# Performance work log

Measured on AMD Instinct MI355X. Metric: run time of the kernel, lower is better.

The kernel has to match this reference:

```python
import jax, jax.numpy as jnp
import numpy as np

N = 50000   # nodes
R = 4       # relation groups
E = 800000  # nnz per relation adjacency
ED = 200000 # decoded edges
H = 128     # hidden_dim
L = 64      # latent_dim
DH = 64     # decoder_hidden_dim


def setup_inputs() -> dict:
    key = jax.random.key(0)
    ks = iter(jax.random.split(key, 64))
    def nrm(shape, scale=1.0):
        return jax.random.normal(next(ks), shape, dtype=jnp.float32) * scale
    inp = {}
    inp["x_process"] = nrm((N, 62))
    inp["x_file"] = nrm((N, 37))
    inp["x_network"] = nrm((N, 37))
    def lin(prefix, din, dout):
        s = 1.0 / np.sqrt(din)
        inp[prefix + "_Ws"] = nrm((dout, din), s)
        inp[prefix + "_bs"] = nrm((dout,), s)
        inp[prefix + "_Wr"] = nrm((R, dout, din), s)
        inp[prefix + "_br"] = nrm((R, dout), s)
    lin("p1", 62, H); lin("p2", H, L)
    lin("f1", 37, H); lin("f2", H, L)
    lin("n1", 37, H); lin("n2", H, L)
    inp["gate_W"] = nrm((3, L), 1.0 / np.sqrt(L))
    inp["gate_b"] = nrm((3,), 0.1)
    inp["dec_W1"] = nrm((DH, 4 * L), 1.0 / np.sqrt(4 * L))
    inp["dec_b1"] = nrm((DH,), 0.1)
    inp["dec_W2"] = nrm((1, DH), 1.0 / np.sqrt(DH))
    inp["dec_b2"] = nrm((1,), 0.1)
    inp["adj_rows"] = jax.random.randint(next(ks), (R, E), 0, N, dtype=jnp.int32)
    inp["adj_cols"] = jax.random.randint(next(ks), (R, E), 0, N, dtype=jnp.int32)
    inp["adj_vals"] = jax.random.uniform(next(ks), (R, E), dtype=jnp.float32) * 0.1
    inp["edge_src"] = jax.random.randint(next(ks), (ED,), 0, N, dtype=jnp.int32)
    inp["edge_dst"] = jax.random.randint(next(ks), (ED,), 0, N, dtype=jnp.int32)
    return inp


def reference(x_process, x_file, x_network,
              p1_Ws, p1_bs, p1_Wr, p1_br, p2_Ws, p2_bs, p2_Wr, p2_br,
              f1_Ws, f1_bs, f1_Wr, f1_br, f2_Ws, f2_bs, f2_Wr, f2_br,
              n1_Ws, n1_bs, n1_Wr, n1_br, n2_Ws, n2_bs, n2_Wr, n2_br,
              gate_W, gate_b, dec_W1, dec_b1, dec_W2, dec_b2,
              adj_rows, adj_cols, adj_vals, edge_src, edge_dst):
    def spmm(rows, cols, vals, x):  # A @ x, A in COO: out[row] += val * x[col]
        return jax.ops.segment_sum(vals[:, None] * x[cols], rows, num_segments=N)

    def rgcn_layer(x, Ws, bs, Wr, br):
        out = x @ Ws.T + bs  # self_linear
        for r in range(R):
            out = out + spmm(adj_rows[r], adj_cols[r], adj_vals[r], x) @ Wr[r].T + br[r]
        return out / float(R + 1)

    def encoder(x, W1s, b1s, W1r, b1r, W2s, b2s, W2r, b2r):
        h = jax.nn.relu(rgcn_layer(x, W1s, b1s, W1r, b1r))
        # dropout p=0.0 / eval mode -> identity
        return rgcn_layer(h, W2s, b2s, W2r, b2r)

    z_p = encoder(x_process, p1_Ws, p1_bs, p1_Wr, p1_br, p2_Ws, p2_bs, p2_Wr, p2_br)
    z_f = encoder(x_file, f1_Ws, f1_bs, f1_Wr, f1_br, f2_Ws, f2_bs, f2_Wr, f2_br)
    z_n = encoder(x_network, n1_Ws, n1_bs, n1_Wr, n1_br, n2_Ws, n2_bs, n2_Wr, n2_br)

    # gated multi-view fusion: three Linear(latent,1) gates -> softmax over views
    scores = jnp.stack([z_p @ gate_W[0] + gate_b[0],
                        z_f @ gate_W[1] + gate_b[1],
                        z_n @ gate_W[2] + gate_b[2]], axis=1)  # [N, 3]
    alpha = jax.nn.softmax(scores, axis=1)
    z = alpha[:, 0:1] * z_p + alpha[:, 1:2] * z_f + alpha[:, 2:3] * z_n  # [N, L]

    # mlp edge decoder
    zs = z[edge_src]
    zd = z[edge_dst]
    feats = jnp.concatenate([zs, zd, zs * zd, jnp.abs(zs - zd)], axis=1)  # [ED, 4L]
    hid = jax.nn.relu(feats @ dec_W1.T + dec_b1)
    logits = (hid @ dec_W2.T + dec_b2)[:, 0]  # [ED]
    return logits
```

## Files before the change

### kernel.cpp

```cpp
#include <hip/hip_runtime.h>

#define N_NODES 50000
#define R_REL   4
#define E_NNZ   800000
#define ED_EDGES 200000
#define H_DIM   128
#define L_DIM   64

#define RN_TOTAL (R_REL * N_NODES)
#define SCAN_BLK 196

#define WS_RP     0u
#define WS_CUR    800256u
#define WS_CNT    1600512u
#define WS_BSUM   2400512u
#define WS_CV     2401536u
#define WS_XALL   28001536u
#define WS_SP     47201536u
#define WS_SF     96801536u
#define WS_SN     126401536u
#define WS_HP     156001536u
#define WS_HF     181601536u
#define WS_HN     47201536u
#define WS_YSP    72801536u
#define WS_YRP    96801536u
#define WS_YSF    122401536u
#define WS_YRF    135201536u
#define WS_YSN    160801536u
#define WS_YRN    173601536u
#define WS_Z      199201536u

__device__ __forceinline__ ushort f2bf(float f) {
    unsigned u = __float_as_uint(f);
    unsigned r = (u + 0x7fffu + ((u >> 16) & 1u)) >> 16;
    return (ushort)r;
}
__device__ __forceinline__ float bf2f(ushort u) {
    return __uint_as_float(((unsigned)u) << 16);
}

__global__ void cast_xall_kernel(const float* __restrict__ xp, const float* __restrict__ xf,
                                 const float* __restrict__ xn, ushort* __restrict__ xall) {
    int i = blockIdx.x * 256 + threadIdx.x;
    if (i >= N_NODES * 192) return;
    int node = i / 192, k = i - node * 192;
    float v = 0.f;
    if (k < 62) v = xp[node * 62 + k];
    else if (k >= 64 && k < 138) {
        int j = k - 64, d = j >> 1;
        v = (j & 1) ? xn[node * 37 + d] : xf[node * 37 + d];
    }
    xall[i] = f2bf(v);
}

__global__ void zero_kernel(int* p, int n) {
    int i = blockIdx.x * blockDim.x + threadIdx.x;
    if (i < n) p[i] = 0;
}

__global__ void hist_kernel(const int* __restrict__ rows, int* __restrict__ counts) {
    int g = blockIdx.x * blockDim.x + threadIdx.x;
    if (g >= R_REL * E_NNZ) return;
    int r = g / E_NNZ;
    atomicAdd(&counts[r * N_NODES + rows[g]], 1);
}

__global__ void scan_part_kernel(const int* __restrict__ counts, int* __restrict__ bsum) {
    __shared__ int red[256];
    int base = blockIdx.x * 1024;
    int t = threadIdx.x;
    int s = 0;
    #pragma unroll
    for (int i = 0; i < 4; i++) {
        int idx = base + i * 256 + t;
        if (idx < RN_TOTAL) s += counts[idx];
    }
    red[t] = s; __syncthreads();
    for (int d = 128; d > 0; d >>= 1) {
        if (t < d) red[t] += red[t + d];
        __syncthreads();
    }
    if (t == 0) bsum[blockIdx.x] = red[0];
}

__global__ void scan_bsum_kernel(int* __restrict__ bsum, int* __restrict__ rp) {
    __shared__ int sh[256];
    int t = threadIdx.x;
    int v = (t < SCAN_BLK) ? bsum[t] : 0;
    sh[t] = v; __syncthreads();
    for (int d = 1; d < 256; d <<= 1) {
        int u = (t >= d) ? sh[t - d] : 0;
        __syncthreads();
        sh[t] += u;
        __syncthreads();
    }
    if (t < SCAN_BLK) bsum[t] = sh[t] - v;
    if (t == 255) rp[RN_TOTAL] = sh[255];
}

__global__ void scan_final_kernel(const int* __restrict__ counts, const int* __restrict__ bsum,
                                  int* __restrict__ rp, int* __restrict__ cursor) {
    __shared__ int sh[256];
    int base = blockIdx.x * 1024;
    int t = threadIdx.x;
    int c[4]; int s = 0;
    #pragma unroll
    for (int i = 0; i < 4; i++) {
        int idx = base + t * 4 + i;
        c[i] = (idx < RN_TOTAL) ? counts[idx] : 0;
        s += c[i];
    }
    sh[t] = s; __syncthreads();
    for (int d = 1; d < 256; d <<= 1) {
        int u = (t >= d) ? sh[t - d] : 0;
        __syncthreads();
        sh[t] += u;
        __syncthreads();
    }
    int off = bsum[blockIdx.x] + sh[t] - s;
    #pragma unroll
    for (int i = 0; i < 4; i++) {
        int idx = base + t * 4 + i;
        if (idx < RN_TOTAL) { rp[idx] = off; cursor[idx] = off; }
        off += c[i];
    }
}

__global__ void scatter_kernel(const int* __restrict__ rows, const int* __restrict__ cols,
                               const float* __restrict__ vals, int* __restrict__ cursor,
                               int2* __restrict__ cse) {
    int g = blockIdx.x * blockDim.x + threadIdx.x;
    if (g >= R_REL * E_NNZ) return;
    int r = g / E_NNZ;
    int p = atomicAdd(&cursor[r * N_NODES + rows[g]], 1);
    cse[p] = make_int2(cols[g], __float_as_int(vals[g]));
}

__global__ void spmm1_all_kernel(const ushort* __restrict__ xall,
                                 const int* __restrict__ rp, const int2* __restrict__ cse,
                                 float* __restrict__ Sp, float* __restrict__ Sf,
                                 float* __restrict__ Sn) {
    int wave = threadIdx.x >> 6, lane = threadIdx.x & 63;
    int row = blockIdx.x * 4 + wave;
    if (row >= N_NODES) return;
    bool lp = lane < 62, lf = lane < 37;
    int opx = lane;
    int ofn = 64 + 2 * lane;
    for (int r = 0; r < R_REL; r++) {
        int e0 = rp[r * N_NODES + row], e1 = rp[r * N_NODES + row + 1];
        float ap = 0.f, af = 0.f, an = 0.f;
        int e = e0;
        for (; e + 4 <= e1; e += 4) {
            int2 q0 = cse[e], q1 = cse[e + 1], q2 = cse[e + 2], q3 = cse[e + 3];
            const ushort* b0 = xall + (size_t)q0.x * 192;
            const ushort* b1 = xall + (size_t)q1.x * 192;
            const ushort* b2 = xall + (size_t)q2.x * 192;
            const ushort* b3 = xall + (size_t)q3.x * 192;
            ushort  p0 = b0[opx], p1 = b1[opx], p2 = b2[opx], p3 = b3[opx];
            ushort2 u0 = *(const ushort2*)&b0[ofn];
            ushort2 u1 = *(const ushort2*)&b1[ofn];
            ushort2 u2 = *(const ushort2*)&b2[ofn];
            ushort2 u3 = *(const ushort2*)&b3[ofn];
            float v0 = __int_as_float(q0.y), v1 = __int_as_float(q1.y);
            float v2 = __int_as_float(q2.y), v3 = __int_as_float(q3.y);
            ap += v0 * bf2f(p0) + v1 * bf2f(p1) + v2 * bf2f(p2) + v3 * bf2f(p3);
            af += v0 * bf2f(u0.x) + v1 * bf2f(u1.x) + v2 * bf2f(u2.x) + v3 * bf2f(u3.x);
            an += v0 * bf2f(u0.y) + v1 * bf2f(u1.y) + v2 * bf2f(u2.y) + v3 * bf2f(u3.y);
        }
        for (; e < e1; e++) {
            int2 q = cse[e];
            const ushort* b = xall + (size_t)q.x * 192;
            float v = __int_as_float(q.y);
            ap += v * bf2f(b[opx]);
            ushort2 u = *(const ushort2*)&b[ofn];
            af += v * bf2f(u.x);
            an += v * bf2f(u.y);
        }
        if (lp) Sp[row * 248 + r * 62 + lane] = ap;
        if (lf) { Sf[row * 148 + r * 37 + lane] = af; Sn[row * 148 + r * 37 + lane] = an; }
    }
}

__launch_bounds__(256)
__global__ void gemm1_kernel(const float* __restrict__ x, const float* __restrict__ S,
                             const float* __restrict__ Ws, const float* __restrict__ bs,
                             const float* __restrict__ Wr, const float* __restrict__ br,
                             float* __restrict__ h, int din) {
    __shared__ float sA[64 * 63];
    __shared__ float sW[62 * 132];
    int t = threadIdx.x;
    int i0 = blockIdx.x * 64;
    int rg = t >> 5, cg = t & 31;
    float acc[8][4] = {};
    for (int s = 0; s < 5; s++) {
        const float* Aptr; int astride;
        if (s == 0) { Aptr = x; astride = din; }
        else        { Aptr = S + (s - 1) * din; astride = 4 * din; }
        const float* Wp = (s == 0) ? Ws : (Wr + (s - 1) * H_DIM * din);
        __syncthreads();
        for (int idx = t; idx < 64 * din; idx += 256) {
            int rr = idx / din, k = idx - rr * din;
            int grow = i0 + rr;
            sA[rr * 63 + k] = (grow < N_NODES) ? Aptr[grow * astride + k] : 0.f;
        }
        for (int idx = t; idx < H_DIM * din; idx += 256) {
            int j = idx / din, k = idx - j * din;
            sW[k * 132 + j] = Wp[j * din + k];
        }
        __syncthreads();
        for (int k = 0; k < din; k++) {
            float a[8];
            #pragma unroll
            for (int rr = 0; rr < 8; rr++) a[rr] = sA[(rg * 8 + rr) * 63 + k];
            float4 w = *(const float4*)&sW[k * 132 + cg * 4];
            #pragma unroll
            for (int rr = 0; rr < 8; rr++) {
                acc[rr][0] += a[rr] * w.x; acc[rr][1] += a[rr] * w.y;
                acc[rr][2] += a[rr] * w.z; acc[rr][3] += a[rr] * w.w;
            }
        }
    }
    int j0 = cg * 4;
    float btot[4];
    #pragma unroll
    for (int cc = 0; cc < 4; cc++) {
        float b = bs[j0 + cc];
        #pragma unroll
        for (int r = 0; r < R_REL; r++) b += br[r * H_DIM + j0 + cc];
        btot[cc] = b;
    }
    #pragma unroll
    for (int rr = 0; rr < 8; rr++) {
        int grow = i0 + rg * 8 + rr;
        if (grow < N_NODES) {
            float4 o;
            o.x = fmaxf((acc[rr][0] + btot[0]) * 0.2f, 0.f);
            o.y = fmaxf((acc[rr][1] + btot[1]) * 0.2f, 0.f);
            o.z = fmaxf((acc[rr][2] + btot[2]) * 0.2f, 0.f);
            o.w = fmaxf((acc[rr][3] + btot[3]) * 0.2f, 0.f);
            *(float4*)&h[grow * H_DIM + j0] = o;
        }
    }
}

__launch_bounds__(256)
__global__ void gemm2_kernel(const float* __restrict__ h, const float* __restrict__ Ws2,
                             const float* __restrict__ Wr2, float* __restrict__ Yself,
                             ushort* __restrict__ Yrel) {
    __shared__ float sA[128 * 65];
    __shared__ float sW[64 * 68];
    int t = threadIdx.x;
    int i0 = blockIdx.x * 128;
    int ct = blockIdx.y;
    int rg = t >> 4, cg = t & 15;
    const float* Wp = (ct == 0) ? Ws2 : (Wr2 + (ct - 1) * 64 * H_DIM);
    float acc[8][4] = {};
    for (int kc = 0; kc < 2; kc++) {
        __syncthreads();
        for (int idx = t; idx < 128 * 64; idx += 256) {
            int rr = idx >> 6, k = idx & 63;
            int grow = i0 + rr;
            sA[rr * 65 + k] = (grow < N_NODES) ? h[grow * H_DIM + kc * 64 + k] : 0.f;
        }
        for (int idx = t; idx < 64 * 64; idx += 256) {
            int j = idx >> 6, k = idx & 63;
            sW[k * 68 + j] = Wp[j * H_DIM + kc * 64 + k];
        }
        __syncthreads();
        for (int k = 0; k < 64; k++) {
            float a[8];
            #pragma unroll
            for (int rr = 0; rr < 8; rr++) a[rr] = sA[(rg * 8 + rr) * 65 + k];
            float4 w = *(const float4*)&sW[k * 68 + cg * 4];
            #pragma unroll
            for (int rr = 0; rr < 8; rr++) {
                acc[rr][0] += a[rr] * w.x; acc[rr][1] += a[rr] * w.y;
                acc[rr][2] += a[rr] * w.z; acc[rr][3] += a[rr] * w.w;
            }
        }
    }
    #pragma unroll
    for (int rr = 0; rr < 8; rr++) {
        int grow = i0 + rg * 8 + rr;
        if (grow < N_NODES) {
            if (ct == 0) {
                float4 o = make_float4(acc[rr][0], acc[rr][1], acc[rr][2], acc[rr][3]);
                *(float4*)&Yself[(size_t)grow * 64 + cg * 4] = o;
            } else {
                ushort4 o;
                o.x = f2bf(acc[rr][0]); o.y = f2bf(acc[rr][1]);
                o.z = f2bf(acc[rr][2]); o.w = f2bf(acc[rr][3]);
                *(ushort4*)&Yrel[(size_t)grow * 256 + (ct - 1) * 64 + cg * 4] = o;
            }
        }
    }
}

__global__ void spmm2z_all_kernel(const float* __restrict__ Ysp, const ushort* __restrict__ Yrp,
                                  const float* __restrict__ Ysf, const ushort* __restrict__ Yrf,
                                  const float* __restrict__ Ysn, const ushort* __restrict__ Yrn,
                                  const int* __restrict__ rp, const int2* __restrict__ cse,
                                  const float* __restrict__ p_bs, const float* __restrict__ p_br,
                                  const float* __restrict__ f_bs, const float* __restrict__ f_br,
                                  const float* __restrict__ n_bs, const float* __restrict__ n_br,
                                  const float* __restrict__ gW, const float* __restrict__ gb,
                                  float* __restrict__ z) {
    int wave = threadIdx.x >> 6, lane = threadIdx.x & 63;
    int row = blockIdx.x * 4 + wave;
    if (row >= N_NODES) return;
    float aP = Ysp[(size_t)row * 64 + lane] + p_bs[lane]
             + p_br[lane] + p_br[64 + lane] + p_br[128 + lane] + p_br[192 + lane];
    float aF = Ysf[(size_t)row * 64 + lane] + f_bs[lane]
             + f_br[lane] + f_br[64 + lane] + f_br[128 + lane] + f_br[192 + lane];
    float aN = Ysn[(size_t)row * 64 + lane] + n_bs[lane]
             + n_br[lane] + n_br[64 + lane] + n_br[128 + lane] + n_br[192 + lane];
    for (int r = 0; r < R_REL; r++) {
        int e0 = rp[r * N_NODES + row], e1 = rp[r * N_NODES + row + 1];
        const ushort* yp = Yrp + r * 64 + lane;
        const ushort* yf = Yrf + r * 64 + lane;
        const ushort* yn = Yrn + r * 64 + lane;
        int e = e0;
        for (; e + 4 <= e1; e += 4) {
            int2 q0 = cse[e], q1 = cse[e + 1], q2 = cse[e + 2], q3 = cse[e + 3];
            size_t o0 = (size_t)q0.x * 256, o1 = (size_t)q1.x * 256;
            size_t o2 = (size_t)q2.x * 256, o3 = (size_t)q3.x * 256;
            float pp0 = bf2f(yp[o0]), pp1 = bf2f(yp[o1]), pp2 = bf2f(yp[o2]), pp3 = bf2f(yp[o3]);
            float ff0 = bf2f(yf[o0]), ff1 = bf2f(yf[o1]), ff2 = bf2f(yf[o2]), ff3 = bf2f(yf[o3]);
            float nn0 = bf2f(yn[o0]), nn1 = bf2f(yn[o1]), nn2 = bf2f(yn[o2]), nn3 = bf2f(yn[o3]);
            float v0 = __int_as_float(q0.y), v1 = __int_as_float(q1.y);
            float v2 = __int_as_float(q2.y), v3 = __int_as_float(q3.y);
            aP += v0 * pp0 + v1 * pp1 + v2 * pp2 + v3 * pp3;
            aF += v0 * ff0 + v1 * ff1 + v2 * ff2 + v3 * ff3;
            aN += v0 * nn0 + v1 * nn1 + v2 * nn2 + v3 * nn3;
        }
        for (; e < e1; e++) {
            int2 q = cse[e];
            size_t o = (size_t)q.x * 256;
            float v = __int_as_float(q.y);
            aP += v * bf2f(yp[o]);
            aF += v * bf2f(yf[o]);
            aN += v * bf2f(yn[o]);
        }
    }
    aP *= 0.2f; aF *= 0.2f; aN *= 0.2f;
    float sp = aP * gW[lane], sf = aF * gW[64 + lane], sn = aN * gW[128 + lane];
    #pragma unroll
    for (int d = 32; d >= 1; d >>= 1) {
        sp += __shfl_xor(sp, d);
        sf += __shfl_xor(sf, d);
        sn += __shfl_xor(sn, d);
    }
    sp += gb[0]; sf += gb[1]; sn += gb[2];
    float m = fmaxf(sp, fmaxf(sf, sn));
    float ep = __expf(sp - m), ef = __expf(sf - m), en = __expf(sn - m);
    float inv = 1.f / (ep + ef + en);
    z[row * 64 + lane] = (ep * aP + ef * aF + en * aN) * inv;
}

__launch_bounds__(256)
__global__ void decoder_kernel(const float* __restrict__ z, const int* __restrict__ esrc,
                               const int* __restrict__ edst, const float* __restrict__ w1,
                               const float* __restrict__ b1, const float* __restrict__ w2,
                               const float* __restrict__ b2, float* __restrict__ out) {
    int e = blockIdx.x * blockDim.x + threadIdx.x;
    if (e >= ED_EDGES) return;
    const float* zs = z + (size_t)esrc[e] * 64;
    const float* zd = z + (size_t)edst[e] * 64;
    float hid[64];
    #pragma unroll
    for (int j = 0; j < 64; j++) hid[j] = b1[j];
    #pragma unroll 1
    for (int kc = 0; kc < 64; kc += 8) {
        float a[8], b[8], p[8], q[8];
        #pragma unroll
        for (int kk = 0; kk < 8; kk++) {
            a[kk] = zs[kc + kk]; b[kk] = zd[kc + kk];
            p[kk] = a[kk] * b[kk]; q[kk] = fabsf(a[kk] - b[kk]);
        }
        #pragma unroll
        for (int j = 0; j < 64; j++) {
            const float* wrow = w1 + j * 256 + kc;
            float s = hid[j];
            #pragma unroll
            for (int kk = 0; kk < 8; kk++) {
                s += a[kk] * wrow[kk] + b[kk] * wrow[64 + kk]
                   + p[kk] * wrow[128 + kk] + q[kk] * wrow[192 + kk];
            }
            hid[j] = s;
        }
    }
    float logit = b2[0];
    #pragma unroll
    for (int j = 0; j < 64; j++) logit += fmaxf(hid[j], 0.f) * w2[j];
    out[e] = logit;
}

extern "C" void kernel_launch(void* const* d_in, const int* in_sizes, int n_in,
                              void* d_out, int out_size, void* d_ws, size_t ws_size,
                              hipStream_t stream) {
    const float* x_p = (const float*)d_in[0];
    const float* x_f = (const float*)d_in[1];
    const float* x_n = (const float*)d_in[2];
    const float* p1_Ws = (const float*)d_in[3];  const float* p1_bs = (const float*)d_in[4];
    const float* p1_Wr = (const float*)d_in[5];  const float* p1_br = (const float*)d_in[6];
    const float* p2_Ws = (const float*)d_in[7];  const float* p2_bs = (const float*)d_in[8];
    const float* p2_Wr = (const float*)d_in[9];  const float* p2_br = (const float*)d_in[10];
    const float* f1_Ws = (const float*)d_in[11]; const float* f1_bs = (const float*)d_in[12];
    const float* f1_Wr = (const float*)d_in[13]; const float* f1_br = (const float*)d_in[14];
    const float* f2_Ws = (const float*)d_in[15]; const float* f2_bs = (const float*)d_in[16];
    const float* f2_Wr = (const float*)d_in[17]; const float* f2_br = (const float*)d_in[18];
    const float* n1_Ws = (const float*)d_in[19]; const float* n1_bs = (const float*)d_in[20];
    const float* n1_Wr = (const float*)d_in[21]; const float* n1_br = (const float*)d_in[22];
    const float* n2_Ws = (const float*)d_in[23]; const float* n2_bs = (const float*)d_in[24];
    const float* n2_Wr = (const float*)d_in[25]; const float* n2_br = (const float*)d_in[26];
    const float* gate_W = (const float*)d_in[27]; const float* gate_b = (const float*)d_in[28];
    const float* dec_W1 = (const float*)d_in[29]; const float* dec_b1 = (const float*)d_in[30];
    const float* dec_W2 = (const float*)d_in[31]; const float* dec_b2 = (const float*)d_in[32];
    const int*   adj_rows = (const int*)d_in[33];
    const int*   adj_cols = (const int*)d_in[34];
    const float* adj_vals = (const float*)d_in[35];
    const int*   edge_src = (const int*)d_in[36];
    const int*   edge_dst = (const int*)d_in[37];

    char* ws = (char*)d_ws;
    int*    rp      = (int*)(ws + WS_RP);
    int*    cursor  = (int*)(ws + WS_CUR);
    int*    counts  = (int*)(ws + WS_CNT);
    int*    bsum    = (int*)(ws + WS_BSUM);
    int2*   cse     = (int2*)(ws + WS_CV);
    ushort* xall    = (ushort*)(ws + WS_XALL);
    float*  S_p = (float*)(ws + WS_SP);
    float*  S_f = (float*)(ws + WS_SF);
    float*  S_n = (float*)(ws + WS_SN);
    float*  h_p = (float*)(ws + WS_HP);
    float*  h_f = (float*)(ws + WS_HF);
    float*  h_n = (float*)(ws + WS_HN);
    float*  Ys_p = (float*)(ws + WS_YSP);  ushort* Yr_p = (ushort*)(ws + WS_YRP);
    float*  Ys_f = (float*)(ws + WS_YSF);  ushort* Yr_f = (ushort*)(ws + WS_YRF);
    float*  Ys_n = (float*)(ws + WS_YSN);  ushort* Yr_n = (ushort*)(ws + WS_YRN);
    float*  z   = (float*)(ws + WS_Z);
    float*  out = (float*)d_out;

    cast_xall_kernel<<<(N_NODES * 192 + 255) / 256, 256, 0, stream>>>(x_p, x_f, x_n, xall);

    zero_kernel<<<(RN_TOTAL + 255) / 256, 256, 0, stream>>>(counts, RN_TOTAL);
    hist_kernel<<<(R_REL * E_NNZ + 255) / 256, 256, 0, stream>>>(adj_rows, counts);
    scan_part_kernel<<<SCAN_BLK, 256, 0, stream>>>(counts, bsum);
    scan_bsum_kernel<<<1, 256, 0, stream>>>(bsum, rp);
    scan_final_kernel<<<SCAN_BLK, 256, 0, stream>>>(counts, bsum, rp, cursor);
    scatter_kernel<<<(R_REL * E_NNZ + 255) / 256, 256, 0, stream>>>(
        adj_rows, adj_cols, adj_vals, cursor, cse);

    spmm1_all_kernel<<<N_NODES / 4, 256, 0, stream>>>(xall, rp, cse, S_p, S_f, S_n);

    int g1 = (N_NODES + 63) / 64;
    gemm1_kernel<<<g1, 256, 0, stream>>>(x_p, S_p, p1_Ws, p1_bs, p1_Wr, p1_br, h_p, 62);
    gemm1_kernel<<<g1, 256, 0, stream>>>(x_f, S_f, f1_Ws, f1_bs, f1_Wr, f1_br, h_f, 37);
    gemm1_kernel<<<g1, 256, 0, stream>>>(x_n, S_n, n1_Ws, n1_bs, n1_Wr, n1_br, h_n, 37);

    dim3 g2((N_NODES + 127) / 128, 5);
    gemm2_kernel<<<g2, 256, 0, stream>>>(h_p, p2_Ws, p2_Wr, Ys_p, Yr_p);
    gemm2_kernel<<<g2, 256, 0, stream>>>(h_f, f2_Ws, f2_Wr, Ys_f, Yr_f);
    gemm2_kernel<<<g2, 256, 0, stream>>>(h_n, n2_Ws, n2_Wr, Ys_n, Yr_n);

    spmm2z_all_kernel<<<N_NODES / 4, 256, 0, stream>>>(
        Ys_p, Yr_p, Ys_f, Yr_f, Ys_n, Yr_n, rp, cse,
        p2_bs, p2_br, f2_bs, f2_br, n2_bs, n2_br, gate_W, gate_b, z);

    decoder_kernel<<<(ED_EDGES + 255) / 256, 256, 0, stream>>>(
        z, edge_src, edge_dst, dec_W1, dec_b1, dec_W2, dec_b2, out);
}
```

Measured before the change: 1.684 ms.

## Replace global-atomic COO-to-CSR build with two-pass LDS radix bucket sort

Builds the CSR adjacency with a two-level sort instead of global atomic histogram and scatter. The first pass buckets edges by relation and the high bits of the row using per-block shared-memory histograms. A prefix scan and scatter then fill a temp buffer, and a per-bucket kernel sorts by the low 8 row bits in LDS and writes row pointers and CSR entries. The aim is to cut contended global atomics and random scattered writes, at the cost of an extra pass through a temp buffer and more workspace aliasing.

```diff
diff --git a/kernel.cpp b/kernel.cpp
--- a/kernel.cpp
+++ b/kernel.cpp
@@ -8,27 +8,35 @@
 #define L_DIM   64
 
 #define RN_TOTAL (R_REL * N_NODES)
-#define SCAN_BLK 196
-
-#define WS_RP     0u
-#define WS_CUR    800256u
-#define WS_CNT    1600512u
-#define WS_BSUM   2400512u
-#define WS_CV     2401536u
-#define WS_XALL   28001536u
-#define WS_SP     47201536u
-#define WS_SF     96801536u
-#define WS_SN     126401536u
-#define WS_HP     156001536u
-#define WS_HF     181601536u
-#define WS_HN     47201536u
-#define WS_YSP    72801536u
-#define WS_YRP    96801536u
-#define WS_YSF    122401536u
-#define WS_YRF    135201536u
-#define WS_YSN    160801536u
-#define WS_YRN    173601536u
-#define WS_Z      199201536u
+#define ETOT     (R_REL * E_NNZ)
+
+#define EPB   8192
+#define NB    391
+#define RBK   196
+#define KBK   (R_REL * RBK)
+#define HTOT  (KBK * NB)
+#define SCB   300
+#define MAXB  6144
+
+#define WS_RP    0u
+#define WS_HIST  800256u
+#define WS_BSUM  2026496u
+#define WS_CV    2030592u
+#define WS_TMP   27630720u
+#define WS_XALL  53230720u
+#define WS_SP    72430720u
+#define WS_SF    122030720u
+#define WS_SN    151630720u
+#define WS_HPR   181230720u
+#define WS_HN    WS_TMP
+#define WS_HF    WS_SP
+#define WS_YSP   WS_XALL
+#define WS_YSF   (WS_SP + 25600000u)
+#define WS_YRP   WS_SF
+#define WS_YRF   WS_SN
+#define WS_YSN   WS_HPR
+#define WS_YRN   WS_HF
+#define WS_Z     194030720u
 
 __device__ __forceinline__ ushort f2bf(float f) {
     unsigned u = __float_as_uint(f);
@@ -53,27 +61,32 @@
     xall[i] = f2bf(v);
 }
 
-__global__ void zero_kernel(int* p, int n) {
-    int i = blockIdx.x * blockDim.x + threadIdx.x;
-    if (i < n) p[i] = 0;
-}
-
-__global__ void hist_kernel(const int* __restrict__ rows, int* __restrict__ counts) {
-    int g = blockIdx.x * blockDim.x + threadIdx.x;
-    if (g >= R_REL * E_NNZ) return;
-    int r = g / E_NNZ;
-    atomicAdd(&counts[r * N_NODES + rows[g]], 1);
-}
-
-__global__ void scan_part_kernel(const int* __restrict__ counts, int* __restrict__ bsum) {
+__global__ void radix_hist_kernel(const int* __restrict__ rows, int* __restrict__ H) {
+    __shared__ int hist[KBK];
+    int blk = blockIdx.x, t = threadIdx.x;
+    for (int i = t; i < KBK; i += 256) hist[i] = 0;
+    __syncthreads();
+    int base = blk * EPB;
+    #pragma unroll 1
+    for (int i = 0; i < EPB / 256; i++) {
+        int g = base + i * 256 + t;
+        if (g < ETOT) {
+            int r = g / E_NNZ;
+            atomicAdd(&hist[r * RBK + (rows[g] >> 8)], 1);
+        }
+    }
+    __syncthreads();
+    for (int i = t; i < KBK; i += 256) H[i * NB + blk] = hist[i];
+}
+
+__global__ void scan_part_kernel(const int* __restrict__ H, int* __restrict__ bsum) {
     __shared__ int red[256];
-    int base = blockIdx.x * 1024;
-    int t = threadIdx.x;
+    int base = blockIdx.x * 1024, t = threadIdx.x;
     int s = 0;
     #pragma unroll
     for (int i = 0; i < 4; i++) {
         int idx = base + i * 256 + t;
-        if (idx < RN_TOTAL) s += counts[idx];
+        if (idx < HTOT) s += H[idx];
     }
     red[t] = s; __syncthreads();
     for (int d = 128; d > 0; d >>= 1) {
@@ -84,30 +97,28 @@
 }
 
 __global__ void scan_bsum_kernel(int* __restrict__ bsum, int* __restrict__ rp) {
+    __shared__ int sh[512];
+    int t = threadIdx.x;
+    int v = (t < SCB) ? bsum[t] : 0;
+    sh[t] = v; __syncthreads();
+    for (int d = 1; d < 512; d <<= 1) {
+        int u = (t >= d) ? sh[t - d] : 0;
+        __syncthreads();
+        sh[t] += u;
+        __syncthreads();
+    }
+    if (t < SCB) bsum[t] = sh[t] - v;
+    if (t == 0) rp[RN_TOTAL] = ETOT;
+}
+
+__global__ void scan_final_kernel(int* __restrict__ H, const int* __restrict__ bsum) {
     __shared__ int sh[256];
-    int t = threadIdx.x;
-    int v = (t < SCAN_BLK) ? bsum[t] : 0;
-    sh[t] = v; __syncthreads();
-    for (int d = 1; d < 256; d <<= 1) {
-        int u = (t >= d) ? sh[t - d] : 0;
-        __syncthreads();
-        sh[t] += u;
-        __syncthreads();
-    }
-    if (t < SCAN_BLK) bsum[t] = sh[t] - v;
-    if (t == 255) rp[RN_TOTAL] = sh[255];
-}
-
-__global__ void scan_final_kernel(const int* __restrict__ counts, const int* __restrict__ bsum,
-                                  int* __restrict__ rp, int* __restrict__ cursor) {
-    __shared__ int sh[256];
-    int base = blockIdx.x * 1024;
-    int t = threadIdx.x;
+    int base = blockIdx.x * 1024, t = threadIdx.x;
     int c[4]; int s = 0;
     #pragma unroll
     for (int i = 0; i < 4; i++) {
         int idx = base + t * 4 + i;
-        c[i] = (idx < RN_TOTAL) ? counts[idx] : 0;
+        c[i] = (idx < HTOT) ? H[idx] : 0;
         s += c[i];
     }
     sh[t] = s; __syncthreads();
@@ -121,19 +132,71 @@
     #pragma unroll
     for (int i = 0; i < 4; i++) {
         int idx = base + t * 4 + i;
-        if (idx < RN_TOTAL) { rp[idx] = off; cursor[idx] = off; }
+        if (idx < HTOT) H[idx] = off;
         off += c[i];
     }
 }
 
-__global__ void scatter_kernel(const int* __restrict__ rows, const int* __restrict__ cols,
-                               const float* __restrict__ vals, int* __restrict__ cursor,
-                               int2* __restrict__ cse) {
-    int g = blockIdx.x * blockDim.x + threadIdx.x;
-    if (g >= R_REL * E_NNZ) return;
-    int r = g / E_NNZ;
-    int p = atomicAdd(&cursor[r * N_NODES + rows[g]], 1);
-    cse[p] = make_int2(cols[g], __float_as_int(vals[g]));
+__global__ void radix_scatter_kernel(const int* __restrict__ rows, const int* __restrict__ cols,
+                                     const float* __restrict__ vals, const int* __restrict__ H,
+                                     int2* __restrict__ tmp) {
+    __shared__ int cur[KBK];
+    int blk = blockIdx.x, t = threadIdx.x;
+    for (int i = t; i < KBK; i += 256) cur[i] = H[i * NB + blk];
+    __syncthreads();
+    int base = blk * EPB;
+    #pragma unroll 1
+    for (int i = 0; i < EPB / 256; i++) {
+        int g = base + i * 256 + t;
+        if (g < ETOT) {
+            int r = g / E_NNZ;
+            int row = rows[g];
+            int b = r * RBK + (row >> 8);
+            int p = atomicAdd(&cur[b], 1);
+            tmp[p] = make_int2(cols[g] | ((row & 255) << 16), __float_as_int(vals[g]));
+        }
+    }
+}
+
+__launch_bounds__(256)
+__global__ void bucket_sort_kernel(const int2* __restrict__ tmp, const int* __restrict__ H,
+                                   int* __restrict__ rp, int2* __restrict__ cse) {
+    __shared__ int hist[256];
+    __shared__ int sc[256];
+    __shared__ int cur[256];
+    __shared__ int2 eb[MAXB];
+    int b = blockIdx.x, t = threadIdx.x;
+    int start = H[b * NB];
+    int end = (b == KBK - 1) ? ETOT : H[(b + 1) * NB];
+    int cnt = end - start;
+    bool useLds = (cnt <= MAXB);
+    hist[t] = 0;
+    __syncthreads();
+    for (int i = t; i < cnt; i += 256) {
+        int2 e = tmp[start + i];
+        if (useLds) eb[i] = e;
+        atomicAdd(&hist[(e.x >> 16) & 255], 1);
+    }
+    __syncthreads();
+    sc[t] = hist[t]; __syncthreads();
+    for (int d = 1; d < 256; d <<= 1) {
+        int v = (t >= d) ? sc[t - d] : 0;
+        __syncthreads();
+        sc[t] += v;
+        __syncthreads();
+    }
+    int pref = sc[t] - hist[t];
+    int r = b / RBK, rh = b - r * RBK;
+    int grow = rh * 256 + t;
+    if (grow < N_NODES) rp[r * N_NODES + grow] = start + pref;
+    cur[t] = start + pref;
+    __syncthreads();
+    for (int i = t; i < cnt; i += 256) {
+        int2 e = useLds ? eb[i] : tmp[start + i];
+        int rl = (e.x >> 16) & 255;
+        int p = atomicAdd(&cur[rl], 1);
+        cse[p] = make_int2(e.x & 0xFFFF, e.y);
+    }
 }
 
 __global__ void spmm1_all_kernel(const ushort* __restrict__ xall,
@@ -423,16 +486,16 @@
     const int*   edge_dst = (const int*)d_in[37];
 
     char* ws = (char*)d_ws;
-    int*    rp      = (int*)(ws + WS_RP);
-    int*    cursor  = (int*)(ws + WS_CUR);
-    int*    counts  = (int*)(ws + WS_CNT);
-    int*    bsum    = (int*)(ws + WS_BSUM);
-    int2*   cse     = (int2*)(ws + WS_CV);
-    ushort* xall    = (ushort*)(ws + WS_XALL);
+    int*    rp   = (int*)(ws + WS_RP);
+    int*    H    = (int*)(ws + WS_HIST);
+    int*    bsum = (int*)(ws + WS_BSUM);
+    int2*   cse  = (int2*)(ws + WS_CV);
+    int2*   tmp  = (int2*)(ws + WS_TMP);
+    ushort* xall = (ushort*)(ws + WS_XALL);
     float*  S_p = (float*)(ws + WS_SP);
     float*  S_f = (float*)(ws + WS_SF);
     float*  S_n = (float*)(ws + WS_SN);
-    float*  h_p = (float*)(ws + WS_HP);
+    float*  h_p = (float*)(ws + WS_HPR);
     float*  h_f = (float*)(ws + WS_HF);
     float*  h_n = (float*)(ws + WS_HN);
     float*  Ys_p = (float*)(ws + WS_YSP);  ushort* Yr_p = (ushort*)(ws + WS_YRP);
@@ -443,13 +506,12 @@
 
     cast_xall_kernel<<<(N_NODES * 192 + 255) / 256, 256, 0, stream>>>(x_p, x_f, x_n, xall);
 
-    zero_kernel<<<(RN_TOTAL + 255) / 256, 256, 0, stream>>>(counts, RN_TOTAL);
-    hist_kernel<<<(R_REL * E_NNZ + 255) / 256, 256, 0, stream>>>(adj_rows, counts);
-    scan_part_kernel<<<SCAN_BLK, 256, 0, stream>>>(counts, bsum);
-    scan_bsum_kernel<<<1, 256, 0, stream>>>(bsum, rp);
-    scan_final_kernel<<<SCAN_BLK, 256, 0, stream>>>(counts, bsum, rp, cursor);
-    scatter_kernel<<<(R_REL * E_NNZ + 255) / 256, 256, 0, stream>>>(
-        adj_rows, adj_cols, adj_vals, cursor, cse);
+    radix_hist_kernel<<<NB, 256, 0, stream>>>(adj_rows, H);
+    scan_part_kernel<<<SCB, 256, 0, stream>>>(H, bsum);
+    scan_bsum_kernel<<<1, 512, 0, stream>>>(bsum, rp);
+    scan_final_kernel<<<SCB, 256, 0, stream>>>(H, bsum);
+    radix_scatter_kernel<<<NB, 256, 0, stream>>>(adj_rows, adj_cols, adj_vals, H, tmp);
+    bucket_sort_kernel<<<KBK, 256, 0, stream>>>(tmp, H, rp, cse);
 
     spmm1_all_kernel<<<N_NODES / 4, 256, 0, stream>>>(xall, rp, cse, S_p, S_f, S_n);
 
```

Result: faster. 1.429 ms (-15.2%).
